# Optimization experiments

Measured on AMD Instinct MI355X. Metric: run time of the kernel, lower is better.

Reference implementation:

```python
import math
import jax, jax.numpy as jnp
import numpy as np

# Dims (match init_kwargs)
B, S, HID = 2, 2048, 2048
H, KVH, D = 16, 8, 128
ATTN_H = 8                      # softmax heads (head_split_dict)
TN_H = H - ATTN_H               # linear (tnorm) heads
N_REP = H // KVH                # GQA repeat factor
FIRST_TOKENS, LAST_TOKENS = 64, 512  # global prefix + band width for custom mask
EPS = 1e-6
ROPE_BASE = 1e6
SCALE = 1.0 / math.sqrt(D)


def _rope_tables(seq_len):
    inv_freq = 1.0 / (ROPE_BASE ** (jnp.arange(0, D, 2, dtype=jnp.float32) / D))
    t = jnp.arange(seq_len, dtype=jnp.float32)
    freqs = jnp.outer(t, inv_freq)                 # [S, D/2]
    emb = jnp.concatenate([freqs, freqs], axis=-1)  # [S, D]
    return jnp.cos(emb), jnp.sin(emb)


def _rotate_half(x):
    x1, x2 = jnp.split(x, 2, axis=-1)
    return jnp.concatenate([-x2, x1], axis=-1)


def _apply_rope(x, cos, sin):
    # x: [B, h, S, D], cos/sin: [S, D]
    return x * cos[None, None] + _rotate_half(x) * sin[None, None]


def _rms_norm(x):
    # SimpleRMSNorm: computed in fp32, no learned weight
    xf = x.astype(jnp.float32)
    out = xf * jax.lax.rsqrt(jnp.mean(xf * xf, axis=-1, keepdims=True) + EPS)
    return out.astype(x.dtype)


def setup_inputs() -> dict:
    key = jax.random.key(0)
    ks = jax.random.split(key, 6)
    sc = 0.02
    perm_np = np.array([3, 7, 0, 12, 9, 15, 1, 5, 2, 4, 6, 8, 10, 11, 13, 14], np.int32)
    inv_np = np.zeros(H, np.int32)
    inv_np[perm_np] = np.arange(H, dtype=np.int32)
    return {
        'hidden_states': jax.random.normal(ks[0], (B, S, HID), jnp.float32),
        'q_w': jax.random.normal(ks[1], (HID, HID), jnp.float32) * sc,
        'q_b': jnp.zeros((HID,), jnp.float32),
        'k_w': jax.random.normal(ks[2], (KVH * D, HID), jnp.float32) * sc,
        'k_b': jnp.zeros((KVH * D,), jnp.float32),
        'v_w': jax.random.normal(ks[3], (KVH * D, HID), jnp.float32) * sc,
        'v_b': jnp.zeros((KVH * D,), jnp.float32),
        'o_w': jax.random.normal(ks[4], (HID, HID), jnp.float32) * sc,
        'head_policy': jnp.array([1, 0, 1, 0, 1, 0, 1, 0], dtype=bool),
        'perm': jnp.asarray(perm_np),
        'inv_perm': jnp.asarray(inv_np),
    }


def _custom_mask(head_policy):
    # create_custom_causal_mask: banded causal + global prefix for heads with
    # policy==False; plain causal for heads with policy==True. Additive mask.
    qi = jnp.arange(S)[:, None]
    ki = jnp.arange(S)[None, :]
    causal = ki <= qi
    band = causal & ((qi - ki) < LAST_TOKENS)
    band = band | ((ki < FIRST_TOKENS) & (qi >= FIRST_TOKENS))
    neg = jnp.finfo(jnp.float32).min
    orig = jnp.where(causal, 0.0, neg)
    new = jnp.where(band, 0.0, neg)
    return jnp.where(head_policy[:, None, None], orig, new), causal  # [ATTN_H,S,S]


def reference(hidden_states, q_w, q_b, k_w, k_b, v_w, v_b, o_w,
              head_policy, perm, inv_perm):
    dt = hidden_states.dtype
    q = hidden_states @ q_w.T + q_b           # [B,S,HID]
    k = hidden_states @ k_w.T + k_b           # [B,S,KVH*D]
    v = hidden_states @ v_w.T + v_b

    # head permutation on q, then split softmax vs tnorm heads
    q = q.reshape(B, S, H, D)[:, :, perm, :]
    q = jnp.transpose(q, (0, 2, 1, 3))        # [B,H,S,D]
    kh = jnp.transpose(k.reshape(B, S, KVH, D), (0, 2, 1, 3))  # [B,KVH,S,D]
    vh = jnp.transpose(v.reshape(B, S, KVH, D), (0, 2, 1, 3))

    cos, sin = _rope_tables(S)
    q = _apply_rope(q, cos, sin)              # rope on all q heads (both branches)
    kh = _apply_rope(kh, cos, sin)

    # repeat_kv (GQA) then head permutation
    k_all = jnp.repeat(kh, N_REP, axis=1)[:, perm]  # [B,H,S,D]
    v_all = jnp.repeat(vh, N_REP, axis=1)[:, perm]

    # ---- softmax branch (first ATTN_H heads), custom banded/global mask ----
    mask, causal = _custom_mask(head_policy)
    logits = jnp.einsum('bhqd,bhkd->bhqk', q[:, :ATTN_H], k_all[:, :ATTN_H]) * SCALE
    logits = logits + mask[None]
    probs = jax.nn.softmax(logits.astype(jnp.float32), axis=-1).astype(dt)
    out_sm = jnp.einsum('bhqk,bhkd->bhqd', probs, v_all[:, :ATTN_H])
    out_sm = jnp.transpose(out_sm, (0, 2, 1, 3)).reshape(B, S, ATTN_H * D)

    # ---- linear (tnorm) branch (remaining heads): masked qk^T @ v + RMSNorm ----
    w = jnp.einsum('bhqd,bhkd->bhqk', q[:, ATTN_H:], k_all[:, ATTN_H:]) * SCALE
    w = jnp.where(causal[None, None], w, jnp.zeros((), dt))
    out_tn = jnp.einsum('bhqk,bhkd->bhqd', w, v_all[:, ATTN_H:])
    out_tn = jnp.transpose(out_tn, (0, 2, 1, 3)).reshape(B, S, TN_H * D)
    out_tn = _rms_norm(out_tn)

    # concat heads, undo permutation, output projection
    out = jnp.concatenate([out_sm, out_tn], axis=-1)
    out = out.reshape(B, S, H, D)[:, :, inv_perm, :].reshape(B, S, HID)
    return out @ o_w.T
```

## Files before the change

kernel.cpp:

```cpp
#include <hip/hip_runtime.h>
#include <hip/hip_bf16.h>
#include <stdint.h>

#define AS1 __attribute__((address_space(1)))
#define AS3 __attribute__((address_space(3)))

typedef __bf16 bf16x8 __attribute__((ext_vector_type(8)));
typedef unsigned short u16x8 __attribute__((ext_vector_type(8)));
typedef float f32x4 __attribute__((ext_vector_type(4)));

static __device__ __forceinline__ unsigned short f2bf(float f) {
  unsigned u = __float_as_uint(f);
  u += 0x7fffu + ((u >> 16) & 1u);
  return (unsigned short)(u >> 16);
}
static __device__ __forceinline__ float bf2f(unsigned short h) {
  return __uint_as_float(((unsigned)h) << 16);
}
static __device__ __forceinline__ bf16x8 ld_frag(const unsigned short* p) {
  union { u16x8 u; bf16x8 b; } c;
  c.u = *(const u16x8*)p;
  return c.b;
}
static __device__ __forceinline__ void gload16(const void* g, void* l) {
  __builtin_amdgcn_global_load_lds((AS1 const void*)g, (AS3 void*)l, 16, 0, 0);
}
#define MFMA(a, b, c) __builtin_amdgcn_mfma_f32_16x16x32_bf16(a, b, c, 0, 0, 0)
#define BAR asm volatile("s_barrier" ::: "memory")
#define VM4 asm volatile("s_waitcnt vmcnt(4)" ::: "memory")

__global__ __launch_bounds__(256)
void cvt_all(const float* __restrict__ hs, const float* __restrict__ qw,
             const float* __restrict__ kw, const float* __restrict__ vw,
             unsigned short* __restrict__ hbf, unsigned short* __restrict__ wqkv) {
  long i = (long)blockIdx.x * 256 + threadIdx.x;
  const float* src; unsigned short* dst; long off;
  if (i < 2097152)      { src = hs; dst = hbf;            off = i; }
  else if (i < 3145728) { src = qw; dst = wqkv;           off = i - 2097152; }
  else if (i < 3670016) { src = kw; dst = wqkv + 4194304; off = i - 3145728; }
  else                  { src = vw; dst = wqkv + 6291456; off = i - 3670016; }
  float4 f = *(const float4*)&src[off * 4];
  ushort4 u;
  u.x = f2bf(f.x); u.y = f2bf(f.y); u.z = f2bf(f.z); u.w = f2bf(f.w);
  *(ushort4*)&dst[off * 4] = u;
}

__global__ __launch_bounds__(256)
void cvt4(const float* __restrict__ in, unsigned short* __restrict__ out, long n) {
  long i = ((long)blockIdx.x * 256 + threadIdx.x) * 4;
  if (i >= n) return;
  float4 f = *(const float4*)&in[i];
  ushort4 u;
  u.x = f2bf(f.x); u.y = f2bf(f.y); u.z = f2bf(f.z); u.w = f2bf(f.w);
  *(ushort4*)&out[i] = u;
}

__global__ __launch_bounds__(256)
void rope_apply(unsigned short* __restrict__ qh, unsigned short* __restrict__ kh) {
  long i = (long)blockIdx.x * 256 + threadIdx.x;
  const long QT = (long)2 * 16 * 2048 * 64;
  unsigned short* p; long rem; float outsc;
  if (i < QT) { p = qh; rem = i; outsc = 0.08838834764831845f; }
  else        { p = kh; rem = i - QT; outsc = 1.0f; }
  int j = (int)(rem & 63);
  long row = rem >> 6;
  int s = (int)(row & 2047);
  unsigned short* x = p + row * 128;
  float inv = exp2f(-0.31143075889569023f * (float)j);
  float f = (float)s * inv;
  float sn, c;
  sincosf(f, &sn, &c);
  float x1 = bf2f(x[j]), x2 = bf2f(x[j + 64]);
  x[j]      = f2bf((x1 * c - x2 * sn) * outsc);
  x[j + 64] = f2bf((x2 * c + x1 * sn) * outsc);
}

__global__ __launch_bounds__(512, 2)
void gemm256_qkv(const unsigned short* __restrict__ A,
                 const unsigned short* __restrict__ Bw,
                 const float* __restrict__ qb, const float* __restrict__ kb,
                 const float* __restrict__ vb,
                 unsigned short* __restrict__ qh, unsigned short* __restrict__ kh,
                 unsigned short* __restrict__ vT) {
  constexpr int K = 2048, NT = K / 64, NIT = NT / 2;
  __shared__ alignas(16) unsigned short LDS[65536];
  const int id = blockIdx.x;
  const int lg = (id & 7) * 32 + (id >> 3);
  const int bm = lg >> 4, bn = lg & 15;
  const int tid = threadIdx.x;
  const int wid = tid >> 6, lane = tid & 63;
  const int wr = wid >> 2, wc = wid & 3;
  const int l15 = lane & 15, lhi = lane >> 4;
  const int rsw = (l15 & 7) << 3;
  const int srow0 = wid * 8 + (lane >> 3);
  const int scol = ((lane & 7) ^ (lane >> 3)) * 8;
  const unsigned short* Ag = A + (long)(bm * 256) * K;
  const unsigned short* Bg = Bw + (long)(bn * 256) * K;
  unsigned short* Al = LDS;
  unsigned short* Bl = LDS + 32768;

#define STG(gb, lb, p, h, t) do {                                              \
    int tc = (t) < NT ? (t) : NT - 1;                                          \
    gload16((gb) + (long)((h) * 128 + srow0) * K + tc * 64 + scol,             \
            (lb) + (p) * 16384 + (h) * 8192 + wid * 512);                      \
    gload16((gb) + (long)((h) * 128 + 64 + srow0) * K + tc * 64 + scol,        \
            (lb) + (p) * 16384 + (h) * 8192 + 4096 + wid * 512);               \
  } while (0)

#define LDA(p, mh) do {                                                        \
    _Pragma("unroll") for (int m4 = 0; m4 < 4; ++m4)                           \
    _Pragma("unroll") for (int kk = 0; kk < 2; ++kk)                           \
      afr[m4][kk] = ld_frag(&Al[(p) * 16384 +                                  \
          (wr * 128 + (mh) * 64 + m4 * 16 + l15) * 64 +                        \
          ((kk * 32 + lhi * 8) ^ rsw)]);                                       \
  } while (0)

#define LDB(p, nh) do {                                                        \
    _Pragma("unroll") for (int n2 = 0; n2 < 2; ++n2)                           \
    _Pragma("unroll") for (int kk = 0; kk < 2; ++kk)                           \
      bfr[nh][n2][kk] = ld_frag(&Bl[(p) * 16384 +                              \
          (wc * 64 + (nh) * 32 + n2 * 16 + l15) * 64 +                         \
          ((kk * 32 + lhi * 8) ^ rsw)]);                                       \
  } while (0)

#define QUAD(mh, nh) do {                                                      \
    __builtin_amdgcn_s_setprio(1);                                             \
    _Pragma("unroll") for (int m4 = 0; m4 < 4; ++m4)                           \
    _Pragma("unroll") for (int n2 = 0; n2 < 2; ++n2)                           \
    _Pragma("unroll") for (int kk = 0; kk < 2; ++kk)                           \
      acc[(mh) * 4 + m4][(nh) * 2 + n2] =                                      \
          MFMA(afr[m4][kk], bfr[nh][n2][kk], acc[(mh) * 4 + m4][(nh) * 2 + n2]);\
    __builtin_amdgcn_s_setprio(0);                                             \
  } while (0)

  f32x4 acc[8][4] = {};
  bf16x8 afr[4][2], bfr[2][2][2];

  STG(Bg, Bl, 0, 0, 0); STG(Bg, Bl, 0, 1, 0);
  STG(Ag, Al, 0, 0, 0); STG(Ag, Al, 0, 1, 0);
  STG(Bg, Bl, 1, 0, 1); STG(Bg, Bl, 1, 1, 1);
  VM4; BAR;

  for (int it = 0; it < NIT; ++it) {
    const int T = 2 * it;
    LDA(0, 0); LDB(0, 0); STG(Ag, Al, 1, 0, T + 1);
    BAR; QUAD(0, 0); BAR;
    LDB(0, 1);            STG(Ag, Al, 1, 1, T + 1);
    BAR; QUAD(0, 1); BAR;
    LDA(0, 1);            STG(Bg, Bl, 0, 0, T + 2);
    BAR; QUAD(1, 0); BAR;
                          STG(Bg, Bl, 0, 1, T + 2);
    VM4; BAR; QUAD(1, 1); BAR;
    LDA(1, 0); LDB(1, 0); STG(Ag, Al, 0, 0, T + 2);
    BAR; QUAD(0, 0); BAR;
    LDB(1, 1);            STG(Ag, Al, 0, 1, T + 2);
    BAR; QUAD(0, 1); BAR;
    LDA(1, 1);            STG(Bg, Bl, 1, 0, T + 3);
    BAR; QUAD(1, 0); BAR;
                          STG(Bg, Bl, 1, 1, T + 3);
    VM4; BAR; QUAD(1, 1); BAR;
  }

  const int r0 = bm * 256 + wr * 128, c0 = bn * 256 + wc * 64;
#pragma unroll
  for (int m = 0; m < 8; ++m) {
#pragma unroll
    for (int n = 0; n < 4; ++n) {
#pragma unroll
      for (int j = 0; j < 4; ++j) {
        int row = r0 + m * 16 + lhi * 4 + j;
        int col = c0 + n * 16 + l15;
        float v = acc[m][n][j];
        int b = row >> 11, s = row & 2047;
        if (col < 2048) {
          v += qb[col];
          qh[((long)(b * 16 + (col >> 7)) * 2048 + s) * 128 + (col & 127)] = f2bf(v);
        } else if (col < 3072) {
          int c = col - 2048; v += kb[c];
          kh[((long)(b * 8 + (c >> 7)) * 2048 + s) * 128 + (c & 127)] = f2bf(v);
        } else {
          int c = col - 3072; v += vb[c];
          vT[((long)(b * 8 + (c >> 7)) * 128 + (c & 127)) * 2048 + s] = f2bf(v);
        }
      }
    }
  }
#undef STG
#undef LDA
#undef LDB
#undef QUAD
}

__global__ __launch_bounds__(256, 2)
void gemm_bt(const unsigned short* __restrict__ A,
             const unsigned short* __restrict__ Bw,
             int K, int N, float* __restrict__ Cout) {
  __shared__ alignas(16) unsigned short As[128 * 64];
  __shared__ alignas(16) unsigned short Bs[128 * 64];
  const int bm = blockIdx.x, bn = blockIdx.y;
  const int tid = threadIdx.x;
  const int w = tid >> 6, l = tid & 63;
  const int wm = w >> 1, wn = w & 1;
  const int l15 = l & 15, lhi = l >> 4;
  f32x4 acc[4][4] = {};
  const unsigned short* aptr = A + ((long)(bm * 128 + w * 8 + (l >> 3))) * K + (l & 7) * 8;
  const unsigned short* bptr = Bw + ((long)(bn * 128 + w * 8 + (l >> 3))) * K + (l & 7) * 8;
  unsigned short* asb = &As[w * 8 * 64];
  unsigned short* bsb = &Bs[w * 8 * 64];
  for (int k0 = 0; k0 < K; k0 += 64) {
#pragma unroll
    for (int i = 0; i < 4; ++i) {
      gload16(aptr + (long)i * 32 * K, asb + i * 2048);
      gload16(bptr + (long)i * 32 * K, bsb + i * 2048);
    }
    aptr += 64; bptr += 64;
    __syncthreads();
#pragma unroll
    for (int kk = 0; kk < 2; ++kk) {
      bf16x8 af[4], bfr[4];
#pragma unroll
      for (int m = 0; m < 4; ++m)
        af[m] = ld_frag(&As[(wm * 64 + m * 16 + l15) * 64 + kk * 32 + lhi * 8]);
#pragma unroll
      for (int n = 0; n < 4; ++n)
        bfr[n] = ld_frag(&Bs[(wn * 64 + n * 16 + l15) * 64 + kk * 32 + lhi * 8]);
#pragma unroll
      for (int m = 0; m < 4; ++m)
#pragma unroll
        for (int n = 0; n < 4; ++n)
          acc[m][n] = MFMA(af[m], bfr[n], acc[m][n]);
    }
    __syncthreads();
  }
#pragma unroll
  for (int m = 0; m < 4; ++m)
#pragma unroll
    for (int n = 0; n < 4; ++n)
#pragma unroll
      for (int j = 0; j < 4; ++j) {
        int row = bm * 128 + wm * 64 + m * 16 + lhi * 4 + j;
        int col = bn * 128 + wn * 64 + n * 16 + l15;
        Cout[(long)row * N + col] = acc[m][n][j];
      }
}

__global__ __launch_bounds__(256, 4)
void attn_all(const unsigned short* __restrict__ qheads,
              const unsigned short* __restrict__ kheads,
              const unsigned short* __restrict__ vT,
              unsigned short* __restrict__ aout,
              unsigned short* __restrict__ tnb,
              const int* __restrict__ perm) {
  __shared__ alignas(16) unsigned short Ks[64 * 128];
  __shared__ alignas(16) unsigned short Vs[128 * 64];
  __shared__ alignas(16) unsigned short Ps[4][16 * 64];
  const int q0 = blockIdx.x * 64;
  const int hy = blockIdx.y;
  const int b = blockIdx.z;
  const bool sm = hy < 8;
  const bool banded = sm && ((hy & 1) != 0);
  const int qhd = perm[hy];
  const int kvh = qhd >> 1;
  const int tid = threadIdx.x, w = tid >> 6, l = tid & 63, l15 = l & 15, lhi = l >> 4;
  const unsigned short* Qg = qheads + ((long)(b * 16 + qhd) * 2048 + q0) * 128;
  const unsigned short* Kg = kheads + (long)(b * 8 + kvh) * 2048 * 128;
  const unsigned short* Vg = vT + (long)(b * 8 + kvh) * 128 * 2048;
  bf16x8 qf[4];
#pragma unroll
  for (int c = 0; c < 4; ++c)
    qf[c] = ld_frag(Qg + (w * 16 + l15) * 128 + c * 32 + lhi * 8);
  f32x4 ao[8] = {};
  float lsum[4] = {0.f, 0.f, 0.f, 0.f};
  const int krow = w * 4 + (l >> 4);
  const long kgoff = (long)krow * 128 + (((l & 15) * 8) ^ ((krow & 7) << 3));
  unsigned short* kdst = &Ks[w * 512];
  const int vrow = w * 8 + (l >> 3);
  const long vgoff = (long)vrow * 2048 + (((l & 7) * 8) ^ ((vrow & 7) << 3));
  unsigned short* vdst = &Vs[w * 512];
  const int rsw15 = (l15 & 7) << 3;

  for (int k0 = 0; k0 <= q0; k0 += 64) {
    if (banded && k0 >= 64 && q0 - k0 >= 575) continue;
    __syncthreads();
#pragma unroll
    for (int p = 0; p < 4; ++p)
      gload16(Kg + (long)(k0 + p * 16) * 128 + kgoff, kdst + p * 2048);
#pragma unroll
    for (int p = 0; p < 4; ++p)
      gload16(Vg + (long)p * 32 * 2048 + k0 + vgoff, vdst + p * 2048);
    __syncthreads();
    f32x4 sacc[4] = {};
    __builtin_amdgcn_s_setprio(1);
#pragma unroll
    for (int c = 0; c < 4; ++c) {
#pragma unroll
      for (int ks = 0; ks < 4; ++ks) {
        bf16x8 kf = ld_frag(&Ks[(ks * 16 + l15) * 128 + ((c * 32 + lhi * 8) ^ rsw15)]);
        sacc[ks] = MFMA(qf[c], kf, sacc[ks]);
      }
    }
    __builtin_amdgcn_s_setprio(0);
    const int qrb = q0 + w * 16 + lhi * 4;
#pragma unroll
    for (int j = 0; j < 4; ++j) {
      const int q = qrb + j;
      const int prow = lhi * 4 + j;
      const int psw = (prow & 7) << 3;
#pragma unroll
      for (int ks = 0; ks < 4; ++ks) {
        int k = k0 + ks * 16 + l15;
        bool ok = (k <= q) && (!banded || k < 64 || (q - k) < 512);
        float p;
        if (sm) { p = ok ? __expf(sacc[ks][j]) : 0.f; lsum[j] += p; }
        else    { p = ok ? sacc[ks][j] : 0.f; }
        Ps[w][prow * 64 + ((ks * 16 + l15) ^ psw)] = f2bf(p);
      }
    }
    bf16x8 pa0 = ld_frag(&Ps[w][l15 * 64 + ((lhi * 8) ^ rsw15)]);
    bf16x8 pa1 = ld_frag(&Ps[w][l15 * 64 + ((32 + lhi * 8) ^ rsw15)]);
    __builtin_amdgcn_s_setprio(1);
#pragma unroll
    for (int n = 0; n < 8; ++n) {
      bf16x8 vf0 = ld_frag(&Vs[(n * 16 + l15) * 64 + ((lhi * 8) ^ rsw15)]);
      bf16x8 vf1 = ld_frag(&Vs[(n * 16 + l15) * 64 + ((32 + lhi * 8) ^ rsw15)]);
      ao[n] = MFMA(pa0, vf0, ao[n]);
      ao[n] = MFMA(pa1, vf1, ao[n]);
    }
    __builtin_amdgcn_s_setprio(0);
  }
  if (sm) {
#pragma unroll
    for (int j = 0; j < 4; ++j) {
      float s = lsum[j];
#pragma unroll
      for (int d = 1; d < 16; d <<= 1) s += __shfl_xor(s, d);
      float inv = 1.0f / s;
      int q = q0 + w * 16 + lhi * 4 + j;
      unsigned short* o = aout + ((long)b * 2048 + q) * 2048 + qhd * 128;
#pragma unroll
      for (int n = 0; n < 8; ++n) o[n * 16 + l15] = f2bf(ao[n][j] * inv);
    }
  } else {
    const int hidx = hy - 8;
#pragma unroll
    for (int j = 0; j < 4; ++j) {
      int q = q0 + w * 16 + lhi * 4 + j;
      unsigned short* o = tnb + ((long)b * 2048 + q) * 1024 + hidx * 128;
#pragma unroll
      for (int n = 0; n < 8; ++n) o[n * 16 + l15] = f2bf(ao[n][j]);
    }
  }
}

__global__ __launch_bounds__(256)
void rms_scatter(const unsigned short* __restrict__ tnb,
                 unsigned short* __restrict__ aout,
                 const int* __restrict__ perm) {
  __shared__ float wsum[4];
  int row = blockIdx.x, tid = threadIdx.x;
  const unsigned short* x = tnb + (long)row * 1024;
  ushort4 u = *(const ushort4*)&x[tid * 4];
  float v0 = bf2f(u.x), v1 = bf2f(u.y), v2 = bf2f(u.z), v3 = bf2f(u.w);
  float ss = v0 * v0 + v1 * v1 + v2 * v2 + v3 * v3;
#pragma unroll
  for (int d = 1; d < 64; d <<= 1) ss += __shfl_xor(ss, d);
  if ((tid & 63) == 0) wsum[tid >> 6] = ss;
  __syncthreads();
  float tot = wsum[0] + wsum[1] + wsum[2] + wsum[3];
  float r = rsqrtf(tot * (1.0f / 1024.0f) + 1e-6f);
  int slot = perm[8 + (tid >> 5)];
  unsigned short* o = aout + (long)row * 2048 + slot * 128 + ((tid * 4) & 127);
  o[0] = f2bf(v0 * r); o[1] = f2bf(v1 * r); o[2] = f2bf(v2 * r); o[3] = f2bf(v3 * r);
}

extern "C" void kernel_launch(void* const* d_in, const int* in_sizes, int n_in,
                              void* d_out, int out_size, void* d_ws, size_t ws_size,
                              hipStream_t stream) {
  const float* hs  = (const float*)d_in[0];
  const float* q_w = (const float*)d_in[1];
  const float* q_b = (const float*)d_in[2];
  const float* k_w = (const float*)d_in[3];
  const float* k_b = (const float*)d_in[4];
  const float* v_w = (const float*)d_in[5];
  const float* v_b = (const float*)d_in[6];
  const float* o_w = (const float*)d_in[7];
  const int* perm  = (const int*)d_in[9];

  char* ws = (char*)d_ws;
  unsigned short* hbf  = (unsigned short*)(ws + 0);
  unsigned short* wqkv = (unsigned short*)(ws + 16777216);
  unsigned short* kh   = (unsigned short*)(ws + 33554432);
  unsigned short* vT   = (unsigned short*)(ws + 41943040);
  unsigned short* qh   = (unsigned short*)d_out;
  unsigned short* aout = hbf;
  unsigned short* tnb  = wqkv;
  unsigned short* owb  = kh;
  float* outF = (float*)d_out;

  cvt_all<<<16384, 256, 0, stream>>>(hs, q_w, k_w, v_w, hbf, wqkv);
  gemm256_qkv<<<256, 512, 0, stream>>>(hbf, wqkv, q_b, k_b, v_b, qh, kh, vT);
  rope_apply<<<24576, 256, 0, stream>>>(qh, kh);
  attn_all<<<dim3(32, 16, 2), 256, 0, stream>>>(qh, kh, vT, aout, tnb, perm);
  cvt4<<<4096, 256, 0, stream>>>(o_w, owb, 4194304);
  rms_scatter<<<4096, 256, 0, stream>>>(tnb, aout, perm);
  gemm_bt<<<dim3(32, 16), 256, 0, stream>>>(aout, owb, 2048, 2048, outF);
}
```

Before: 279.4 us.

## Prefetch next K/V tile into registers while computing current tile

Replaces the synchronous global-to-LDS K/V copy at the top of each key-block iteration with a register-staged software pipeline. The next tile is loaded into registers before the QK^T and PV MFMAs run, then written to LDS between two barriers after compute. The banded-head skip logic moves into a next-block function that jumps straight past the masked-out middle region instead of iterating and continuing. This aims to hide global load latency behind matrix work, at the cost of about 32 extra VGPRs per thread, which may lower occupancy.

```diff
diff --git a/kernel.cpp b/kernel.cpp
--- a/kernel.cpp
+++ b/kernel.cpp
@@ -273,22 +273,36 @@
   float lsum[4] = {0.f, 0.f, 0.f, 0.f};
   const int krow = w * 4 + (l >> 4);
   const long kgoff = (long)krow * 128 + (((l & 15) * 8) ^ ((krow & 7) << 3));
-  unsigned short* kdst = &Ks[w * 512];
   const int vrow = w * 8 + (l >> 3);
   const long vgoff = (long)vrow * 2048 + (((l & 7) * 8) ^ ((vrow & 7) << 3));
-  unsigned short* vdst = &Vs[w * 512];
+  unsigned short* kwr = &Ks[w * 512 + l * 8];
+  unsigned short* vwr = &Vs[w * 512 + l * 8];
   const int rsw15 = (l15 & 7) << 3;
 
-  for (int k0 = 0; k0 <= q0; k0 += 64) {
-    if (banded && k0 >= 64 && q0 - k0 >= 575) continue;
-    __syncthreads();
-#pragma unroll
-    for (int p = 0; p < 4; ++p)
-      gload16(Kg + (long)(k0 + p * 16) * 128 + kgoff, kdst + p * 2048);
-#pragma unroll
-    for (int p = 0; p < 4; ++p)
-      gload16(Vg + (long)p * 32 * 2048 + k0 + vgoff, vdst + p * 2048);
-    __syncthreads();
+  u16x8 kst[4], vst[4];
+#define LOADT(k0) do {                                                         \
+    _Pragma("unroll") for (int p = 0; p < 4; ++p)                              \
+      kst[p] = *(const u16x8*)(Kg + (long)((k0) + p * 16) * 128 + kgoff);      \
+    _Pragma("unroll") for (int p = 0; p < 4; ++p)                              \
+      vst[p] = *(const u16x8*)(Vg + (long)p * 32 * 2048 + (k0) + vgoff);       \
+  } while (0)
+#define WRT do {                                                               \
+    _Pragma("unroll") for (int p = 0; p < 4; ++p)                              \
+      *(u16x8*)(kwr + p * 2048) = kst[p];                                      \
+    _Pragma("unroll") for (int p = 0; p < 4; ++p)                              \
+      *(u16x8*)(vwr + p * 2048) = vst[p];                                      \
+  } while (0)
+#define NXT(k0) ((banded && (q0 - ((k0) + 64)) >= 575 && ((k0) + 64) >= 64)    \
+                     ? (q0 - 512) : ((k0) + 64))
+
+  LOADT(0);
+  WRT;
+  __syncthreads();
+  int k0 = 0;
+  for (;;) {
+    const int k1 = NXT(k0);
+    const bool more = (k1 <= q0);
+    if (more) LOADT(k1);
     f32x4 sacc[4] = {};
     __builtin_amdgcn_s_setprio(1);
 #pragma unroll
@@ -327,7 +341,16 @@
       ao[n] = MFMA(pa1, vf1, ao[n]);
     }
     __builtin_amdgcn_s_setprio(0);
+    if (!more) break;
+    __syncthreads();
+    WRT;
+    __syncthreads();
+    k0 = k1;
   }
+#undef LOADT
+#undef WRT
+#undef NXT
+
   if (sm) {
 #pragma unroll
     for (int j = 0; j < 4; ++j) {
```

After: 336.3 us. 1.2x slower.

## Split long causal attention rows into two KV halves with combine pass

Applied to the files above, without the earlier changes.

For the non-banded heads, query tiles in the second half of the sequence are split into two KV-range slices, each computed by its own block, and the partial outputs and row sums are written to scratch. A new combine kernel adds the slices and normalises them. Block indices are reversed so the heaviest tiles launch first. The aim is to balance load across the causal triangle and shorten the tail, at the cost of an extra kernel, scratch traffic and bf16 rounding of the partial sums. The softmax path uses no running max, so adding the partials directly stays consistent with the original math.

```diff
diff --git a/kernel.cpp b/kernel.cpp
--- a/kernel.cpp
+++ b/kernel.cpp
@@ -250,15 +250,30 @@
               const unsigned short* __restrict__ vT,
               unsigned short* __restrict__ aout,
               unsigned short* __restrict__ tnb,
+              unsigned short* __restrict__ pao0, unsigned short* __restrict__ pao1,
+              float* __restrict__ pl0, float* __restrict__ pl1,
               const int* __restrict__ perm) {
   __shared__ alignas(16) unsigned short Ks[64 * 128];
   __shared__ alignas(16) unsigned short Vs[128 * 64];
   __shared__ alignas(16) unsigned short Ps[4][16 * 64];
-  const int q0 = blockIdx.x * 64;
+  const int bx = 47 - blockIdx.x;
   const int hy = blockIdx.y;
   const int b = blockIdx.z;
   const bool sm = hy < 8;
   const bool banded = sm && ((hy & 1) != 0);
+  int t, kst, ket;
+  bool partial = false, slice1 = false;
+  if (banded) {
+    if (bx >= 32) return;
+    t = bx; kst = 0; ket = t;
+  } else if (bx < 16) {
+    t = bx; kst = 0; ket = t;
+  } else if (bx < 32) {
+    t = bx; int h = (t + 2) >> 1; kst = 0; ket = h - 1; partial = true;
+  } else {
+    t = bx - 16; int h = (t + 2) >> 1; kst = h; ket = t; partial = true; slice1 = true;
+  }
+  const int q0 = t * 64;
   const int qhd = perm[hy];
   const int kvh = qhd >> 1;
   const int tid = threadIdx.x, w = tid >> 6, l = tid & 63, l15 = l & 15, lhi = l >> 4;
@@ -279,7 +294,7 @@
   unsigned short* vdst = &Vs[w * 512];
   const int rsw15 = (l15 & 7) << 3;
 
-  for (int k0 = 0; k0 <= q0; k0 += 64) {
+  for (int k0 = kst * 64; k0 <= ket * 64; k0 += 64) {
     if (banded && k0 >= 64 && q0 - k0 >= 575) continue;
     __syncthreads();
 #pragma unroll
@@ -328,7 +343,26 @@
     }
     __builtin_amdgcn_s_setprio(0);
   }
-  if (sm) {
+
+  if (partial) {
+    const int hc = sm ? (hy >> 1) : (hy - 4);
+    const long rbase = (long)(b * 12 + hc) * 1024 + (q0 - 1024);
+    unsigned short* pb = (slice1 ? pao1 : pao0) + rbase * 128;
+    float* plb = (slice1 ? pl1 : pl0) + rbase;
+#pragma unroll
+    for (int j = 0; j < 4; ++j) {
+      const int r = w * 16 + lhi * 4 + j;
+      if (sm) {
+        float s = lsum[j];
+#pragma unroll
+        for (int d = 1; d < 16; d <<= 1) s += __shfl_xor(s, d);
+        if (l15 == 0) plb[r] = s;
+      }
+#pragma unroll
+      for (int n = 0; n < 8; ++n)
+        pb[(long)r * 128 + n * 16 + l15] = f2bf(ao[n][j]);
+    }
+  } else if (sm) {
 #pragma unroll
     for (int j = 0; j < 4; ++j) {
       float s = lsum[j];
@@ -349,6 +383,29 @@
 #pragma unroll
       for (int n = 0; n < 8; ++n) o[n * 16 + l15] = f2bf(ao[n][j]);
     }
+  }
+}
+
+__global__ __launch_bounds__(256)
+void combine(const unsigned short* __restrict__ pao0,
+             const unsigned short* __restrict__ pao1,
+             const float* __restrict__ pl0, const float* __restrict__ pl1,
+             unsigned short* __restrict__ aout, unsigned short* __restrict__ tnb,
+             const int* __restrict__ perm) {
+  long i = (long)blockIdx.x * 256 + threadIdx.x;
+  long row = i >> 7;
+  int col = (int)(i & 127);
+  int b = (int)(row / 12288);
+  int rem = (int)(row - (long)b * 12288);
+  int hc = rem >> 10;
+  int q = 1024 + (rem & 1023);
+  float a = bf2f(pao0[i]) + bf2f(pao1[i]);
+  if (hc < 4) {
+    int qhd = perm[hc * 2];
+    float lv = pl0[row] + pl1[row];
+    aout[((long)b * 2048 + q) * 2048 + qhd * 128 + col] = f2bf(a / lv);
+  } else {
+    tnb[((long)b * 2048 + q) * 1024 + (hc - 4) * 128 + col] = f2bf(a);
   }
 }
 
@@ -391,7 +448,12 @@
   unsigned short* wqkv = (unsigned short*)(ws + 16777216);
   unsigned short* kh   = (unsigned short*)(ws + 33554432);
   unsigned short* vT   = (unsigned short*)(ws + 41943040);
-  unsigned short* qh   = (unsigned short*)d_out;
+  char* dob = (char*)d_out;
+  unsigned short* qh   = (unsigned short*)dob;
+  unsigned short* pao0 = (unsigned short*)(dob + 16777216);
+  unsigned short* pao1 = (unsigned short*)(dob + 23068672);
+  float* pl0           = (float*)(dob + 29360128);
+  float* pl1           = (float*)(dob + 29458432);
   unsigned short* aout = hbf;
   unsigned short* tnb  = wqkv;
   unsigned short* owb  = kh;
@@ -400,7 +462,9 @@
   cvt_all<<<16384, 256, 0, stream>>>(hs, q_w, k_w, v_w, hbf, wqkv);
   gemm256_qkv<<<256, 512, 0, stream>>>(hbf, wqkv, q_b, k_b, v_b, qh, kh, vT);
   rope_apply<<<24576, 256, 0, stream>>>(qh, kh);
-  attn_all<<<dim3(32, 16, 2), 256, 0, stream>>>(qh, kh, vT, aout, tnb, perm);
+  attn_all<<<dim3(48, 16, 2), 256, 0, stream>>>(qh, kh, vT, aout, tnb,
+                                                pao0, pao1, pl0, pl1, perm);
+  combine<<<12288, 256, 0, stream>>>(pao0, pao1, pl0, pl1, aout, tnb, perm);
   cvt4<<<4096, 256, 0, stream>>>(o_w, owb, 4194304);
   rms_scatter<<<4096, 256, 0, stream>>>(tnb, aout, perm);
   gemm_bt<<<dim3(32, 16), 256, 0, stream>>>(aout, owb, 2048, 2048, outF);
```

Measured after the change: 276.5 us. No clear change (-1.0%).
